# Kernel tuning notes

Measured on AMD Instinct MI355X. Metric: run time of the kernel, lower is better.

Reference implementation:

```python
import jax, jax.numpy as jnp
import numpy as np

B = 65536
NFIELD = 20
NFEAT = 1_000_000
SQL_NEMB = 10
DATA_NEMB = 10
HID = 64
K = 16
C = 2
COL_CARD = NFIELD + NFEAT + 1
GATE_IN = NFIELD * SQL_NEMB
EXP_IN = NFIELD * DATA_NEMB
EPS = 1e-5


def _bn(x, g, b, m, v):
    # eval-mode BatchNorm1d: affine normalize with running stats
    return (x - m) * jax.lax.rsqrt(v + EPS) * g + b


def setup_inputs() -> dict:
    key = jax.random.key(0)
    ks = jax.random.split(key, 12)
    n = lambda k, s, sc=0.05: jax.random.normal(k, s, jnp.float32) * sc
    return {
        "x": jax.random.randint(ks[0], (B, NFIELD), 0, NFEAT, dtype=jnp.int32),
        "sql": jax.random.randint(ks[1], (B, NFIELD), 0, COL_CARD, dtype=jnp.int32),
        "input_table": n(ks[2], (NFEAT, DATA_NEMB)),
        "sql_table": n(ks[3], (COL_CARD, SQL_NEMB)),
        "gate_w1": n(ks[4], (GATE_IN, HID)), "gate_b1": jnp.zeros((HID,), jnp.float32),
        "gate_w2": n(ks[5], (HID, K)), "gate_b2": jnp.zeros((K,), jnp.float32),
        "e_w1": n(ks[6], (K, EXP_IN, HID)), "e_b1": jnp.zeros((K, HID), jnp.float32),
        "e_g1": jnp.ones((K, HID), jnp.float32), "e_beta1": jnp.zeros((K, HID), jnp.float32),
        "e_m1": jnp.zeros((K, HID), jnp.float32), "e_v1": jnp.ones((K, HID), jnp.float32),
        "e_w2": n(ks[7], (K, HID, HID)), "e_b2": jnp.zeros((K, HID), jnp.float32),
        "e_g2": jnp.ones((K, HID), jnp.float32), "e_beta2": jnp.zeros((K, HID), jnp.float32),
        "e_m2": jnp.zeros((K, HID), jnp.float32), "e_v2": jnp.ones((K, HID), jnp.float32),
        "p_w1": n(ks[8], (HID, HID)), "p_b1": jnp.zeros((HID,), jnp.float32),
        "p_g": jnp.ones((HID,), jnp.float32), "p_beta": jnp.zeros((HID,), jnp.float32),
        "p_m": jnp.zeros((HID,), jnp.float32), "p_v": jnp.ones((HID,), jnp.float32),
        "p_w2": n(ks[9], (HID, 1)), "p_b2": jnp.zeros((1,), jnp.float32),
    }


def reference(x, sql, input_table, sql_table, gate_w1, gate_b1, gate_w2, gate_b2,
              e_w1, e_b1, e_g1, e_beta1, e_m1, e_v1,
              e_w2, e_b2, e_g2, e_beta2, e_m2, e_v2,
              p_w1, p_b1, p_g, p_beta, p_m, p_v, p_w2, p_b2):
    Bn = x.shape[0]
    # embedding lookups -> flatten fields
    x_emb = input_table[x].reshape(Bn, -1)      # [B, nfield*data_nemb]
    sql_emb = sql_table[sql].reshape(Bn, -1)    # [B, nfield*sql_nemb]
    # gate network (MLP + softmax) over K experts
    gh = jax.nn.relu(sql_emb @ gate_w1 + gate_b1)
    scores = jax.nn.softmax(gh @ gate_w2 + gate_b2, axis=-1)  # [B, K]
    # sparse top-C selection, scatter back to dense gates, renormalize
    topv, topi = jax.lax.top_k(scores, C)
    gates = jnp.zeros_like(scores).at[jnp.arange(Bn)[:, None], topi].set(topv)
    gates = gates / (gates.sum(-1, keepdims=True) + 1e-9)     # [B, K]
    # expert compute (dense-equivalent; zero gates kill unselected experts)
    h1 = jax.nn.relu(_bn(jnp.einsum('bi,kih->kbh', x_emb, e_w1) + e_b1[:, None, :],
                         e_g1[:, None, :], e_beta1[:, None, :], e_m1[:, None, :], e_v1[:, None, :]))
    h2 = jax.nn.relu(_bn(jnp.einsum('kbh,khg->kbg', h1, e_w2) + e_b2[:, None, :],
                         e_g2[:, None, :], e_beta2[:, None, :], e_m2[:, None, :], e_v2[:, None, :]))
    y = jnp.einsum('bk,kbh->bh', gates, h2)                   # combine [B, HID]
    # load-balance loss: cv^2 of expert importance
    importance = gates.sum(0)
    loss = importance.var() / (importance.mean() ** 2 + 1e-10)
    # predict head
    ph = jax.nn.relu(_bn(y @ p_w1 + p_b1, p_g, p_beta, p_m, p_v))
    out = (ph @ p_w2 + p_b2).squeeze(-1)                      # [B]
    return out, loss
```

## Files before the change

kernel.cpp:

```cpp
#include <hip/hip_runtime.h>
#include <hip/hip_bf16.h>

#define BB 65536
#define NFIELD 20
#define HID 64
#define KEXP 16
#define EPS 1e-5f
#define KPAD 224
#define NKS 7
#define NBLK_GATE 256
#define NBX_EXP 40
#define EMB_BPB 16

typedef __attribute__((ext_vector_type(8))) short v8s;
typedef __attribute__((ext_vector_type(4))) float v4f;

#define OFF_GCNT 0
#define OFF_SC1 64
#define OFF_SH1 1088
#define OFF_SC2 2112
#define OFF_SH2 3136
#define OFF_SCP 4160
#define OFF_SHP 4224
#define OFF_IMP 4288
#define OFF_LIDX 8448
#define OFF_LW  1057024
#define OFF_W1T 2105600
#define OFF_GW1T 2220288
#define OFF_W2T 2227456
#define OFF_PW1T 2260224
#define OFF_XEMB 2262272
#define OFF_SQEMB 9602416
#define OFF_HS 16942448

__device__ __forceinline__ unsigned short f2bf(float f) {
    unsigned int u = __float_as_uint(f);
    unsigned int r = (u + 0x7FFFu + ((u >> 16) & 1u)) >> 16;
    return (unsigned short)r;
}
__device__ __forceinline__ float bf2f(unsigned short u) {
    unsigned int t = ((unsigned int)u) << 16;
    return __uint_as_float(t);
}

__global__ __launch_bounds__(256) void k_prep(
    const float* __restrict__ ew1, const float* __restrict__ ew2,
    const float* __restrict__ gw1, const float* __restrict__ pw1,
    const float* __restrict__ eb1, const float* __restrict__ eg1,
    const float* __restrict__ ebe1, const float* __restrict__ em1,
    const float* __restrict__ ev1,
    const float* __restrict__ eb2, const float* __restrict__ eg2,
    const float* __restrict__ ebe2, const float* __restrict__ em2,
    const float* __restrict__ ev2,
    const float* __restrict__ pb1, const float* __restrict__ pg,
    const float* __restrict__ pbe, const float* __restrict__ pm,
    const float* __restrict__ pv,
    float* __restrict__ wsf, int* __restrict__ gcnt,
    unsigned short* __restrict__ w1t, unsigned short* __restrict__ gw1t,
    unsigned short* __restrict__ w2t, unsigned short* __restrict__ pw1t)
{
    int gid = blockIdx.x * 256 + threadIdx.x;
    if (gid < 229376) {
        int k = gid / 14336, r = gid % 14336, c = r / KPAD, t = r % KPAD;
        w1t[gid] = (t < 200) ? f2bf(ew1[((size_t)k * 200 + t) * HID + c]) : 0;
    } else if (gid < 229376 + 14336) {
        int g2 = gid - 229376; int c = g2 / KPAD, t = g2 % KPAD;
        gw1t[g2] = (t < 200) ? f2bf(gw1[t * HID + c]) : 0;
    } else if (gid < 243712 + 65536) {
        int g2 = gid - 243712; int k = g2 / 4096, r = g2 % 4096, g = r / 64, i = r % 64;
        w2t[g2] = f2bf(ew2[((size_t)k * 64 + i) * 64 + g]);
    } else if (gid < 309248 + 4096) {
        int g2 = gid - 309248; int g = g2 / 64, i = g2 % 64;
        pw1t[g2] = f2bf(pw1[i * 64 + g]);
    } else if (gid < 313344 + 1024) {
        int t = gid - 313344;
        float rs1 = rsqrtf(ev1[t] + EPS) * eg1[t];
        wsf[OFF_SC1 + t] = rs1;
        wsf[OFF_SH1 + t] = fmaf(eb1[t] - em1[t], rs1, ebe1[t]);
        float rs2 = rsqrtf(ev2[t] + EPS) * eg2[t];
        wsf[OFF_SC2 + t] = rs2;
        wsf[OFF_SH2 + t] = fmaf(eb2[t] - em2[t], rs2, ebe2[t]);
    } else if (gid < 314368 + 64) {
        int t = gid - 314368;
        float rs = rsqrtf(pv[t] + EPS) * pg[t];
        wsf[OFF_SCP + t] = rs;
        wsf[OFF_SHP + t] = fmaf(pb1[t] - pm[t], rs, pbe[t]);
    } else if (gid < 314432 + 16) {
        gcnt[gid - 314432] = 0;
    }
}

__global__ __launch_bounds__(256) void k_emb(
    const int* __restrict__ x, const int* __restrict__ sql,
    const float* __restrict__ itab, const float* __restrict__ stab,
    unsigned short* __restrict__ xembT, unsigned short* __restrict__ sqembT)
{
    __shared__ unsigned int lbuf[EMB_BPB * 112];
    int blk = blockIdx.x;
    int sel = blk >= (BB / EMB_BPB);
    int b0 = (sel ? blk - (BB / EMB_BPB) : blk) * EMB_BPB;
    const int* idxp = sel ? sql : x;
    const float* tab = sel ? stab : itab;
    unsigned short* dst = sel ? sqembT : xembT;
    int tid = threadIdx.x;

    if (tid < EMB_BPB * 12)
        lbuf[(tid / 12) * 112 + 100 + (tid % 12)] = 0;

    for (int r = tid; r < EMB_BPB * NFIELD; r += 256) {
        int lb = r / NFIELD, f = r % NFIELD;
        int idx = idxp[b0 * NFIELD + r];
        const float* row = tab + (size_t)idx * 10;
        unsigned int* lrow = &lbuf[lb * 112 + f * 5];
        float2 t0 = *(const float2*)(row + 0);
        float2 t1 = *(const float2*)(row + 2);
        float2 t2 = *(const float2*)(row + 4);
        float2 t3 = *(const float2*)(row + 6);
        float2 t4 = *(const float2*)(row + 8);
        lrow[0] = (unsigned int)f2bf(t0.x) | ((unsigned int)f2bf(t0.y) << 16);
        lrow[1] = (unsigned int)f2bf(t1.x) | ((unsigned int)f2bf(t1.y) << 16);
        lrow[2] = (unsigned int)f2bf(t2.x) | ((unsigned int)f2bf(t2.y) << 16);
        lrow[3] = (unsigned int)f2bf(t3.x) | ((unsigned int)f2bf(t3.y) << 16);
        lrow[4] = (unsigned int)f2bf(t4.x) | ((unsigned int)f2bf(t4.y) << 16);
    }
    __syncthreads();
    uint4* g4 = (uint4*)(dst + (size_t)b0 * KPAD);
    const uint4* l4 = (const uint4*)lbuf;
    g4[tid] = l4[tid];
    if (tid < EMB_BPB * 112 / 4 - 256) g4[256 + tid] = l4[256 + tid];
}

__global__ __launch_bounds__(256, 2) void k_gate(
    const unsigned short* __restrict__ sqembT, const unsigned short* __restrict__ gw1t,
    const float* __restrict__ gb1, const float* __restrict__ gw2,
    const float* __restrict__ gb2,
    int* __restrict__ lidx, float* __restrict__ lw,
    int* __restrict__ gcnt, float* __restrict__ imp_part)
{
    __shared__ unsigned short Hg[4][64][80];
    __shared__ float s_imp[KEXP];
    __shared__ int s_cnt[KEXP];
    __shared__ int s_base[KEXP];
    int tid = threadIdx.x;
    int wid = tid >> 6, l = tid & 63;
    int m = l & 15, q = l >> 4;
    if (tid < KEXP) { s_imp[tid] = 0.f; s_cnt[tid] = 0; }
    __syncthreads();

    int it0 = blockIdx.x * 256 + wid * 64;
    v4f zero4 = {0.f, 0.f, 0.f, 0.f};
    v4f acc[4][4];
#pragma unroll
    for (int a = 0; a < 4; ++a)
#pragma unroll
        for (int c = 0; c < 4; ++c) acc[a][c] = zero4;

    const unsigned short* Ab = sqembT + (size_t)it0 * KPAD + q * 8;
    const unsigned short* Bb = gw1t + m * KPAD + q * 8;
#pragma unroll
    for (int Ks = 0; Ks < NKS; ++Ks) {
        v8s a[4], b[4];
#pragma unroll
        for (int Mt = 0; Mt < 4; ++Mt)
            a[Mt] = *(const v8s*)(Ab + (Mt * 16 + m) * KPAD + Ks * 32);
#pragma unroll
        for (int Nt = 0; Nt < 4; ++Nt)
            b[Nt] = *(const v8s*)(Bb + Nt * 16 * KPAD + Ks * 32);
#pragma unroll
        for (int Mt = 0; Mt < 4; ++Mt)
#pragma unroll
            for (int Nt = 0; Nt < 4; ++Nt)
                acc[Mt][Nt] = __builtin_amdgcn_mfma_f32_16x16x32_bf16(a[Mt], b[Nt], acc[Mt][Nt], 0, 0, 0);
    }
#pragma unroll
    for (int Nt = 0; Nt < 4; ++Nt) {
        int c = Nt * 16 + m;
        float bias = gb1[c];
#pragma unroll
        for (int Mt = 0; Mt < 4; ++Mt)
#pragma unroll
            for (int j = 0; j < 4; ++j) {
                int item = Mt * 16 + q * 4 + j;
                float v = fmaxf(acc[Mt][Nt][j] + bias, 0.f);
                Hg[wid][item][c ^ ((item & 7) << 3)] = f2bf(v);
            }
    }
    float z[KEXP];
#pragma unroll
    for (int j = 0; j < KEXP; ++j) z[j] = gb2[j];
#pragma unroll
    for (int u = 0; u < 8; ++u) {
        v8s hv = *(const v8s*)&Hg[wid][l][(u * 8) ^ ((l & 7) << 3)];
#pragma unroll
        for (int e = 0; e < 8; ++e) {
            int h = u * 8 + e;
            float g = bf2f((unsigned short)hv[e]);
#pragma unroll
            for (int j = 0; j < KEXP; ++j) z[j] = fmaf(g, gw2[h * KEXP + j], z[j]);
        }
    }
    float mm = z[0];
#pragma unroll
    for (int j = 1; j < KEXP; ++j) mm = fmaxf(mm, z[j]);
    float s = 0.f;
#pragma unroll
    for (int j = 0; j < KEXP; ++j) s += expf(z[j] - mm);
    int i0 = 0; float m0 = z[0];
#pragma unroll
    for (int j = 1; j < KEXP; ++j) if (z[j] > m0) { m0 = z[j]; i0 = j; }
    int i1 = (i0 == 0) ? 1 : 0; float m1 = -3.4e38f;
#pragma unroll
    for (int j = 0; j < KEXP; ++j) if (j != i0 && z[j] > m1) { m1 = z[j]; i1 = j; }
    float v0 = expf(m0 - mm) / s, v1 = expf(m1 - mm) / s;
    float inv = 1.f / (v0 + v1 + 1e-9f);
    float w0 = v0 * inv, w1 = v1 * inv;

    int b = blockIdx.x * 256 + tid;
    atomicAdd(&s_imp[i0], w0);
    atomicAdd(&s_imp[i1], w1);
    int o0 = atomicAdd(&s_cnt[i0], 1);
    int o1 = atomicAdd(&s_cnt[i1], 1);
    __syncthreads();
    if (tid < KEXP) {
        imp_part[blockIdx.x * KEXP + tid] = s_imp[tid];
        s_base[tid] = atomicAdd(&gcnt[tid], s_cnt[tid]);
    }
    __syncthreads();
    int p0 = i0 * BB + s_base[i0] + o0;
    lidx[p0] = (b << 1);     lw[p0] = w0;
    int p1 = i1 * BB + s_base[i1] + o1;
    lidx[p1] = (b << 1) | 1; lw[p1] = w1;
}

__global__ void k_pad(const int* __restrict__ gcnt, int* __restrict__ lidx,
                      float* __restrict__ lw)
{
    int k = blockIdx.x;
    int n = gcnt[k];
    int ne = (n + 63) & ~63;
    for (int i = n + threadIdx.x; i < ne; i += 64) {
        lidx[k * BB + i] = 2 * BB;
        lw[k * BB + i] = 0.f;
    }
}

__global__ __launch_bounds__(256) void k_loss(const float* __restrict__ imp_part,
                                              float* __restrict__ out)
{
    __shared__ double sred[16][17];
    __shared__ double simp[KEXP];
    int tid = threadIdx.x;
    int j = tid & 15, g = tid >> 4;
    double s = 0.0;
    for (int blk = g; blk < NBLK_GATE; blk += 16) s += (double)imp_part[blk * KEXP + j];
    sred[g][j] = s;
    __syncthreads();
    if (tid < KEXP) {
        double t = 0.0;
#pragma unroll
        for (int gg = 0; gg < 16; ++gg) t += sred[gg][tid];
        simp[tid] = t;
    }
    __syncthreads();
    if (tid == 0) {
        double mean = 0.0;
        for (int jj = 0; jj < KEXP; ++jj) mean += simp[jj];
        mean /= KEXP;
        double var = 0.0;
        for (int jj = 0; jj < KEXP; ++jj) { double d = simp[jj] - mean; var += d * d; }
        var /= KEXP;
        out[BB] = (float)(var / (mean * mean + 1e-10));
    }
}

__global__ __launch_bounds__(256, 2) void k_exp(
    const unsigned short* __restrict__ xembT,
    const unsigned short* __restrict__ w1t, const unsigned short* __restrict__ w2t,
    const float* __restrict__ sc1, const float* __restrict__ sh1,
    const float* __restrict__ sc2, const float* __restrict__ sh2,
    const int* __restrict__ lidx, const float* __restrict__ lw,
    const int* __restrict__ gcnt, unsigned short* __restrict__ hs)
{
    __shared__ unsigned short Hl[4][64][80];
    int k = blockIdx.y;
    int tid = threadIdx.x;
    int wid = tid >> 6, l = tid & 63;
    int m = l & 15, q = l >> 4;
    int n = gcnt[k];
    int ne = (n + 63) & ~63;
    const unsigned short* W1 = w1t + (size_t)k * 64 * KPAD + m * KPAD + q * 8;
    const unsigned short* W2 = w2t + (size_t)k * 64 * 64 + m * 64 + q * 8;
    float sc1v[4], sh1v[4], sc2v[4], sh2v[4];
#pragma unroll
    for (int Nt = 0; Nt < 4; ++Nt) {
        int c = Nt * 16 + m;
        sc1v[Nt] = sc1[k * HID + c]; sh1v[Nt] = sh1[k * HID + c];
        sc2v[Nt] = sc2[k * HID + c]; sh2v[Nt] = sh2[k * HID + c];
    }
    v4f zero4 = {0.f, 0.f, 0.f, 0.f};

    for (int it0 = (blockIdx.x * 4 + wid) * 64; it0 < ne; it0 += NBX_EXP * 256) {
        int eA[4];
#pragma unroll
        for (int Mt = 0; Mt < 4; ++Mt) eA[Mt] = lidx[k * BB + it0 + Mt * 16 + m];
        v4f acc1[4][4];
#pragma unroll
        for (int a = 0; a < 4; ++a)
#pragma unroll
            for (int c = 0; c < 4; ++c) acc1[a][c] = zero4;
#pragma unroll
        for (int Ks = 0; Ks < NKS; ++Ks) {
            v8s a[4], b[4];
#pragma unroll
            for (int Mt = 0; Mt < 4; ++Mt)
                a[Mt] = *(const v8s*)(xembT + (size_t)(eA[Mt] >> 1) * KPAD + Ks * 32 + q * 8);
#pragma unroll
            for (int Nt = 0; Nt < 4; ++Nt)
                b[Nt] = *(const v8s*)(W1 + Nt * 16 * KPAD + Ks * 32);
#pragma unroll
            for (int Mt = 0; Mt < 4; ++Mt)
#pragma unroll
                for (int Nt = 0; Nt < 4; ++Nt)
                    acc1[Mt][Nt] = __builtin_amdgcn_mfma_f32_16x16x32_bf16(a[Mt], b[Nt], acc1[Mt][Nt], 0, 0, 0);
        }
#pragma unroll
        for (int Nt = 0; Nt < 4; ++Nt) {
            int c = Nt * 16 + m;
#pragma unroll
            for (int Mt = 0; Mt < 4; ++Mt)
#pragma unroll
                for (int j = 0; j < 4; ++j) {
                    int item = Mt * 16 + q * 4 + j;
                    float v = fmaxf(fmaf(acc1[Mt][Nt][j], sc1v[Nt], sh1v[Nt]), 0.f);
                    Hl[wid][item][c ^ ((item & 7) << 3)] = f2bf(v);
                }
        }
        v4f acc2[4][4];
#pragma unroll
        for (int a = 0; a < 4; ++a)
#pragma unroll
            for (int c = 0; c < 4; ++c) acc2[a][c] = zero4;
#pragma unroll
        for (int Ks = 0; Ks < 2; ++Ks) {
            v8s a[4], b[4];
#pragma unroll
            for (int Mt = 0; Mt < 4; ++Mt)
                a[Mt] = *(const v8s*)&Hl[wid][Mt * 16 + m][(Ks * 32 + q * 8) ^ ((m & 7) << 3)];
#pragma unroll
            for (int Nt = 0; Nt < 4; ++Nt)
                b[Nt] = *(const v8s*)(W2 + Nt * 16 * 64 + Ks * 32);
#pragma unroll
            for (int Mt = 0; Mt < 4; ++Mt)
#pragma unroll
                for (int Nt = 0; Nt < 4; ++Nt)
                    acc2[Mt][Nt] = __builtin_amdgcn_mfma_f32_16x16x32_bf16(a[Mt], b[Nt], acc2[Mt][Nt], 0, 0, 0);
        }
#pragma unroll
        for (int Mt = 0; Mt < 4; ++Mt) {
            float4 wC = *(const float4*)&lw[k * BB + it0 + Mt * 16 + q * 4];
            float wj[4] = {wC.x, wC.y, wC.z, wC.w};
#pragma unroll
            for (int Nt = 0; Nt < 4; ++Nt) {
                int c = Nt * 16 + m;
#pragma unroll
                for (int j = 0; j < 4; ++j) {
                    int item = Mt * 16 + q * 4 + j;
                    float v = wj[j] * fmaxf(fmaf(acc2[Mt][Nt][j], sc2v[Nt], sh2v[Nt]), 0.f);
                    Hl[wid][item][c ^ ((item & 7) << 3)] = f2bf(v);
                }
            }
        }
        int eo = lidx[k * BB + it0 + l];
        unsigned short* hrow = hs + (size_t)eo * HID;
#pragma unroll
        for (int u = 0; u < 8; ++u)
            *(v8s*)(hrow + u * 8) = *(const v8s*)&Hl[wid][l][(u * 8) ^ ((l & 7) << 3)];
    }
}

__global__ __launch_bounds__(256, 2) void k_head(
    const unsigned short* __restrict__ hs, const unsigned short* __restrict__ pw1t,
    const float* __restrict__ scp, const float* __restrict__ shp,
    const float* __restrict__ pw2, const float* __restrict__ pb2,
    float* __restrict__ out)
{
    int tid = threadIdx.x;
    int wid = tid >> 6, l = tid & 63;
    int m = l & 15, q = l >> 4;
    int it0 = blockIdx.x * 256 + wid * 64;
    float scv[4], shv[4], w2v[4];
#pragma unroll
    for (int Nt = 0; Nt < 4; ++Nt) {
        int c = Nt * 16 + m;
        scv[Nt] = scp[c]; shv[Nt] = shp[c]; w2v[Nt] = pw2[c];
    }
    v4f zero4 = {0.f, 0.f, 0.f, 0.f};
    v4f acc[4][4];
#pragma unroll
    for (int a = 0; a < 4; ++a)
#pragma unroll
        for (int c = 0; c < 4; ++c) acc[a][c] = zero4;

#pragma unroll
    for (int Ks = 0; Ks < 2; ++Ks) {
        v8s a[4], b[4];
#pragma unroll
        for (int Mt = 0; Mt < 4; ++Mt) {
            int bi = it0 + Mt * 16 + m;
            const unsigned short* r0 = hs + (size_t)(2 * bi) * HID + Ks * 32 + q * 8;
            v8s u0 = *(const v8s*)r0;
            v8s u1 = *(const v8s*)(r0 + HID);
            v8s av;
#pragma unroll
            for (int e = 0; e < 8; ++e) {
                float f = bf2f((unsigned short)u0[e]) + bf2f((unsigned short)u1[e]);
                av[e] = (short)f2bf(f);
            }
            a[Mt] = av;
        }
#pragma unroll
        for (int Nt = 0; Nt < 4; ++Nt)
            b[Nt] = *(const v8s*)(pw1t + (Nt * 16 + m) * HID + Ks * 32 + q * 8);
#pragma unroll
        for (int Mt = 0; Mt < 4; ++Mt)
#pragma unroll
            for (int Nt = 0; Nt < 4; ++Nt)
                acc[Mt][Nt] = __builtin_amdgcn_mfma_f32_16x16x32_bf16(a[Mt], b[Nt], acc[Mt][Nt], 0, 0, 0);
    }
    float pb2v = pb2[0];
#pragma unroll
    for (int Mt = 0; Mt < 4; ++Mt) {
#pragma unroll
        for (int j = 0; j < 4; ++j) {
            float po = 0.f;
#pragma unroll
            for (int Nt = 0; Nt < 4; ++Nt) {
                float ph = fmaxf(fmaf(acc[Mt][Nt][j], scv[Nt], shv[Nt]), 0.f);
                po = fmaf(ph, w2v[Nt], po);
            }
            po += __shfl_xor(po, 1);
            po += __shfl_xor(po, 2);
            po += __shfl_xor(po, 4);
            po += __shfl_xor(po, 8);
            if (m == 0) out[it0 + Mt * 16 + q * 4 + j] = po + pb2v;
        }
    }
}

extern "C" void kernel_launch(void* const* d_in, const int* in_sizes, int n_in,
                              void* d_out, int out_size, void* d_ws, size_t ws_size,
                              hipStream_t stream) {
    const int*   x     = (const int*)d_in[0];
    const int*   sql   = (const int*)d_in[1];
    const float* itab  = (const float*)d_in[2];
    const float* stab  = (const float*)d_in[3];
    const float* gw1   = (const float*)d_in[4];
    const float* gb1   = (const float*)d_in[5];
    const float* gw2   = (const float*)d_in[6];
    const float* gb2   = (const float*)d_in[7];
    const float* ew1   = (const float*)d_in[8];
    const float* eb1   = (const float*)d_in[9];
    const float* eg1   = (const float*)d_in[10];
    const float* ebe1  = (const float*)d_in[11];
    const float* em1   = (const float*)d_in[12];
    const float* ev1   = (const float*)d_in[13];
    const float* ew2   = (const float*)d_in[14];
    const float* eb2   = (const float*)d_in[15];
    const float* eg2   = (const float*)d_in[16];
    const float* ebe2  = (const float*)d_in[17];
    const float* em2   = (const float*)d_in[18];
    const float* ev2   = (const float*)d_in[19];
    const float* pw1   = (const float*)d_in[20];
    const float* pb1   = (const float*)d_in[21];
    const float* pg    = (const float*)d_in[22];
    const float* pbe   = (const float*)d_in[23];
    const float* pm    = (const float*)d_in[24];
    const float* pv    = (const float*)d_in[25];
    const float* pw2   = (const float*)d_in[26];
    const float* pb2   = (const float*)d_in[27];

    float* wsf = (float*)d_ws;
    int*   wsi = (int*)d_ws;
    int*   gcnt = wsi + OFF_GCNT;
    float* sc1 = wsf + OFF_SC1;
    float* sh1 = wsf + OFF_SH1;
    float* sc2 = wsf + OFF_SC2;
    float* sh2 = wsf + OFF_SH2;
    float* scp = wsf + OFF_SCP;
    float* shp = wsf + OFF_SHP;
    float* imp = wsf + OFF_IMP;
    int*   lidx = wsi + OFF_LIDX;
    float* lw  = wsf + OFF_LW;
    unsigned short* w1t   = (unsigned short*)(wsf + OFF_W1T);
    unsigned short* gw1t  = (unsigned short*)(wsf + OFF_GW1T);
    unsigned short* w2t   = (unsigned short*)(wsf + OFF_W2T);
    unsigned short* pw1t  = (unsigned short*)(wsf + OFF_PW1T);
    unsigned short* xembT = (unsigned short*)(wsf + OFF_XEMB);
    unsigned short* sqembT= (unsigned short*)(wsf + OFF_SQEMB);
    unsigned short* hs    = (unsigned short*)(wsf + OFF_HS);
    float* out = (float*)d_out;

    k_prep<<<1229, 256, 0, stream>>>(ew1, ew2, gw1, pw1,
                                     eb1, eg1, ebe1, em1, ev1,
                                     eb2, eg2, ebe2, em2, ev2,
                                     pb1, pg, pbe, pm, pv,
                                     wsf, gcnt, w1t, gw1t, w2t, pw1t);
    k_emb<<<2 * (BB / EMB_BPB), 256, 0, stream>>>(x, sql, itab, stab, xembT, sqembT);
    k_gate<<<NBLK_GATE, 256, 0, stream>>>(sqembT, gw1t, gb1, gw2, gb2,
                                          lidx, lw, gcnt, imp);
    k_loss<<<1, 256, 0, stream>>>(imp, out);
    k_pad<<<16, 64, 0, stream>>>(gcnt, lidx, lw);
    dim3 ge(NBX_EXP, KEXP);
    k_exp<<<ge, 256, 0, stream>>>(xembT, w1t, w2t, sc1, sh1, sc2, sh2,
                                  lidx, lw, gcnt, hs);
    k_head<<<256, 256, 0, stream>>>(hs, pw1t, scp, shp, pw2, pb2, out);
}
```

Measured before the change: 153.2 us.

## Fuse SQL embedding gather into gate kernel and drop sqembT buffer

The SQL-table embedding gather moves out of k_emb and into k_gate. Each gate block now gathers its own 64 rows into a shared-memory tile and runs the MFMA GEMM from LDS. Each wave computes 16 hidden columns instead of 64 items, and the grid grows to 1024 blocks. This removes the global write and read-back of the bf16 sqembT intermediate, at the cost of a gather-bound prologue in the gate kernel, a single wave doing softmax/top-k per block, and barriers placed inside divergent branches.

```diff
diff --git a/kernel.cpp b/kernel.cpp
--- a/kernel.cpp
+++ b/kernel.cpp
@@ -8,9 +8,10 @@
 #define EPS 1e-5f
 #define KPAD 224
 #define NKS 7
-#define NBLK_GATE 256
+#define NBLK_GATE 1024
 #define NBX_EXP 40
 #define EMB_BPB 16
+#define TSTR 228
 
 typedef __attribute__((ext_vector_type(8))) short v8s;
 typedef __attribute__((ext_vector_type(4))) float v4f;
@@ -23,15 +24,14 @@
 #define OFF_SCP 4160
 #define OFF_SHP 4224
 #define OFF_IMP 4288
-#define OFF_LIDX 8448
-#define OFF_LW  1057024
-#define OFF_W1T 2105600
-#define OFF_GW1T 2220288
-#define OFF_W2T 2227456
-#define OFF_PW1T 2260224
-#define OFF_XEMB 2262272
-#define OFF_SQEMB 9602416
-#define OFF_HS 16942448
+#define OFF_LIDX 20672
+#define OFF_LW  1069248
+#define OFF_W1T 2117824
+#define OFF_GW1T 2232512
+#define OFF_W2T 2239680
+#define OFF_PW1T 2272448
+#define OFF_XEMB 2274496
+#define OFF_HS 9614640
 
 __device__ __forceinline__ unsigned short f2bf(float f) {
     unsigned int u = __float_as_uint(f);
@@ -91,17 +91,11 @@
 }
 
 __global__ __launch_bounds__(256) void k_emb(
-    const int* __restrict__ x, const int* __restrict__ sql,
-    const float* __restrict__ itab, const float* __restrict__ stab,
-    unsigned short* __restrict__ xembT, unsigned short* __restrict__ sqembT)
+    const int* __restrict__ x, const float* __restrict__ itab,
+    unsigned short* __restrict__ xembT)
 {
     __shared__ unsigned int lbuf[EMB_BPB * 112];
-    int blk = blockIdx.x;
-    int sel = blk >= (BB / EMB_BPB);
-    int b0 = (sel ? blk - (BB / EMB_BPB) : blk) * EMB_BPB;
-    const int* idxp = sel ? sql : x;
-    const float* tab = sel ? stab : itab;
-    unsigned short* dst = sel ? sqembT : xembT;
+    int b0 = blockIdx.x * EMB_BPB;
     int tid = threadIdx.x;
 
     if (tid < EMB_BPB * 12)
@@ -109,8 +103,8 @@
 
     for (int r = tid; r < EMB_BPB * NFIELD; r += 256) {
         int lb = r / NFIELD, f = r % NFIELD;
-        int idx = idxp[b0 * NFIELD + r];
-        const float* row = tab + (size_t)idx * 10;
+        int idx = x[b0 * NFIELD + r];
+        const float* row = itab + (size_t)idx * 10;
         unsigned int* lrow = &lbuf[lb * 112 + f * 5];
         float2 t0 = *(const float2*)(row + 0);
         float2 t1 = *(const float2*)(row + 2);
@@ -124,112 +118,134 @@
         lrow[4] = (unsigned int)f2bf(t4.x) | ((unsigned int)f2bf(t4.y) << 16);
     }
     __syncthreads();
-    uint4* g4 = (uint4*)(dst + (size_t)b0 * KPAD);
+    uint4* g4 = (uint4*)(xembT + (size_t)b0 * KPAD);
     const uint4* l4 = (const uint4*)lbuf;
     g4[tid] = l4[tid];
     if (tid < EMB_BPB * 112 / 4 - 256) g4[256 + tid] = l4[256 + tid];
 }
 
-__global__ __launch_bounds__(256, 2) void k_gate(
-    const unsigned short* __restrict__ sqembT, const unsigned short* __restrict__ gw1t,
+__global__ __launch_bounds__(256) void k_gate(
+    const int* __restrict__ sql, const float* __restrict__ stab,
+    const unsigned short* __restrict__ gw1t,
     const float* __restrict__ gb1, const float* __restrict__ gw2,
     const float* __restrict__ gb2,
     int* __restrict__ lidx, float* __restrict__ lw,
     int* __restrict__ gcnt, float* __restrict__ imp_part)
 {
-    __shared__ unsigned short Hg[4][64][80];
+    __shared__ unsigned short tile[64][TSTR];
     __shared__ float s_imp[KEXP];
     __shared__ int s_cnt[KEXP];
     __shared__ int s_base[KEXP];
+    unsigned short (*Hg)[80] = (unsigned short (*)[80])&tile[0][0];
     int tid = threadIdx.x;
     int wid = tid >> 6, l = tid & 63;
     int m = l & 15, q = l >> 4;
+    int b0 = blockIdx.x * 64;
+
     if (tid < KEXP) { s_imp[tid] = 0.f; s_cnt[tid] = 0; }
-    __syncthreads();
-
-    int it0 = blockIdx.x * 256 + wid * 64;
+    for (int t = tid; t < 64 * 12; t += 256) {
+        int r = t / 12, c2 = t % 12;
+        *(unsigned int*)&tile[r][200 + 2 * c2] = 0;
+    }
+#pragma unroll
+    for (int rr = 0; rr < 5; ++rr) {
+        int r = tid + rr * 256;
+        int lb = r / NFIELD, f = r % NFIELD;
+        int idx = sql[(size_t)(b0 + lb) * NFIELD + f];
+        const float* row = stab + (size_t)idx * 10;
+        float2 t0 = *(const float2*)(row + 0);
+        float2 t1 = *(const float2*)(row + 2);
+        float2 t2 = *(const float2*)(row + 4);
+        float2 t3 = *(const float2*)(row + 6);
+        float2 t4 = *(const float2*)(row + 8);
+        unsigned int* lrow = (unsigned int*)&tile[lb][f * 10];
+        lrow[0] = (unsigned int)f2bf(t0.x) | ((unsigned int)f2bf(t0.y) << 16);
+        lrow[1] = (unsigned int)f2bf(t1.x) | ((unsigned int)f2bf(t1.y) << 16);
+        lrow[2] = (unsigned int)f2bf(t2.x) | ((unsigned int)f2bf(t2.y) << 16);
+        lrow[3] = (unsigned int)f2bf(t3.x) | ((unsigned int)f2bf(t3.y) << 16);
+        lrow[4] = (unsigned int)f2bf(t4.x) | ((unsigned int)f2bf(t4.y) << 16);
+    }
+    __syncthreads();
+
     v4f zero4 = {0.f, 0.f, 0.f, 0.f};
-    v4f acc[4][4];
-#pragma unroll
-    for (int a = 0; a < 4; ++a)
-#pragma unroll
-        for (int c = 0; c < 4; ++c) acc[a][c] = zero4;
-
-    const unsigned short* Ab = sqembT + (size_t)it0 * KPAD + q * 8;
-    const unsigned short* Bb = gw1t + m * KPAD + q * 8;
+    v4f acc[4];
+#pragma unroll
+    for (int a = 0; a < 4; ++a) acc[a] = zero4;
+    const unsigned short* Bb = gw1t + (wid * 16 + m) * KPAD + q * 8;
 #pragma unroll
     for (int Ks = 0; Ks < NKS; ++Ks) {
-        v8s a[4], b[4];
+        v8s bv = *(const v8s*)(Bb + Ks * 32);
+        v8s a[4];
 #pragma unroll
         for (int Mt = 0; Mt < 4; ++Mt)
-            a[Mt] = *(const v8s*)(Ab + (Mt * 16 + m) * KPAD + Ks * 32);
-#pragma unroll
-        for (int Nt = 0; Nt < 4; ++Nt)
-            b[Nt] = *(const v8s*)(Bb + Nt * 16 * KPAD + Ks * 32);
+            a[Mt] = *(const v8s*)&tile[Mt * 16 + m][Ks * 32 + q * 8];
 #pragma unroll
         for (int Mt = 0; Mt < 4; ++Mt)
-#pragma unroll
-            for (int Nt = 0; Nt < 4; ++Nt)
-                acc[Mt][Nt] = __builtin_amdgcn_mfma_f32_16x16x32_bf16(a[Mt], b[Nt], acc[Mt][Nt], 0, 0, 0);
-    }
-#pragma unroll
-    for (int Nt = 0; Nt < 4; ++Nt) {
-        int c = Nt * 16 + m;
-        float bias = gb1[c];
-#pragma unroll
-        for (int Mt = 0; Mt < 4; ++Mt)
-#pragma unroll
-            for (int j = 0; j < 4; ++j) {
-                int item = Mt * 16 + q * 4 + j;
-                float v = fmaxf(acc[Mt][Nt][j] + bias, 0.f);
-                Hg[wid][item][c ^ ((item & 7) << 3)] = f2bf(v);
+            acc[Mt] = __builtin_amdgcn_mfma_f32_16x16x32_bf16(a[Mt], bv, acc[Mt], 0, 0, 0);
+    }
+    __syncthreads();
+
+    int c = wid * 16 + m;
+    float bias = gb1[c];
+#pragma unroll
+    for (int Mt = 0; Mt < 4; ++Mt)
+#pragma unroll
+        for (int j = 0; j < 4; ++j) {
+            int item = Mt * 16 + q * 4 + j;
+            float v = fmaxf(acc[Mt][j] + bias, 0.f);
+            Hg[item][c ^ ((item & 7) << 3)] = f2bf(v);
+        }
+    __syncthreads();
+
+    if (wid == 0) {
+        float z[KEXP];
+#pragma unroll
+        for (int j = 0; j < KEXP; ++j) z[j] = gb2[j];
+#pragma unroll
+        for (int u = 0; u < 8; ++u) {
+            v8s hv = *(const v8s*)&Hg[l][(u * 8) ^ ((l & 7) << 3)];
+#pragma unroll
+            for (int e = 0; e < 8; ++e) {
+                int h = u * 8 + e;
+                float g = bf2f((unsigned short)hv[e]);
+#pragma unroll
+                for (int j = 0; j < KEXP; ++j) z[j] = fmaf(g, gw2[h * KEXP + j], z[j]);
             }
-    }
-    float z[KEXP];
-#pragma unroll
-    for (int j = 0; j < KEXP; ++j) z[j] = gb2[j];
-#pragma unroll
-    for (int u = 0; u < 8; ++u) {
-        v8s hv = *(const v8s*)&Hg[wid][l][(u * 8) ^ ((l & 7) << 3)];
-#pragma unroll
-        for (int e = 0; e < 8; ++e) {
-            int h = u * 8 + e;
-            float g = bf2f((unsigned short)hv[e]);
-#pragma unroll
-            for (int j = 0; j < KEXP; ++j) z[j] = fmaf(g, gw2[h * KEXP + j], z[j]);
-        }
-    }
-    float mm = z[0];
-#pragma unroll
-    for (int j = 1; j < KEXP; ++j) mm = fmaxf(mm, z[j]);
-    float s = 0.f;
-#pragma unroll
-    for (int j = 0; j < KEXP; ++j) s += expf(z[j] - mm);
-    int i0 = 0; float m0 = z[0];
-#pragma unroll
-    for (int j = 1; j < KEXP; ++j) if (z[j] > m0) { m0 = z[j]; i0 = j; }
-    int i1 = (i0 == 0) ? 1 : 0; float m1 = -3.4e38f;
-#pragma unroll
-    for (int j = 0; j < KEXP; ++j) if (j != i0 && z[j] > m1) { m1 = z[j]; i1 = j; }
-    float v0 = expf(m0 - mm) / s, v1 = expf(m1 - mm) / s;
-    float inv = 1.f / (v0 + v1 + 1e-9f);
-    float w0 = v0 * inv, w1 = v1 * inv;
-
-    int b = blockIdx.x * 256 + tid;
-    atomicAdd(&s_imp[i0], w0);
-    atomicAdd(&s_imp[i1], w1);
-    int o0 = atomicAdd(&s_cnt[i0], 1);
-    int o1 = atomicAdd(&s_cnt[i1], 1);
-    __syncthreads();
-    if (tid < KEXP) {
-        imp_part[blockIdx.x * KEXP + tid] = s_imp[tid];
-        s_base[tid] = atomicAdd(&gcnt[tid], s_cnt[tid]);
-    }
-    __syncthreads();
-    int p0 = i0 * BB + s_base[i0] + o0;
-    lidx[p0] = (b << 1);     lw[p0] = w0;
-    int p1 = i1 * BB + s_base[i1] + o1;
-    lidx[p1] = (b << 1) | 1; lw[p1] = w1;
+        }
+        float mm = z[0];
+#pragma unroll
+        for (int j = 1; j < KEXP; ++j) mm = fmaxf(mm, z[j]);
+        float s = 0.f;
+#pragma unroll
+        for (int j = 0; j < KEXP; ++j) s += expf(z[j] - mm);
+        int i0 = 0; float m0 = z[0];
+#pragma unroll
+        for (int j = 1; j < KEXP; ++j) if (z[j] > m0) { m0 = z[j]; i0 = j; }
+        int i1 = (i0 == 0) ? 1 : 0; float m1 = -3.4e38f;
+#pragma unroll
+        for (int j = 0; j < KEXP; ++j) if (j != i0 && z[j] > m1) { m1 = z[j]; i1 = j; }
+        float v0 = expf(m0 - mm) / s, v1 = expf(m1 - mm) / s;
+        float inv = 1.f / (v0 + v1 + 1e-9f);
+        float w0 = v0 * inv, w1 = v1 * inv;
+
+        atomicAdd(&s_imp[i0], w0);
+        atomicAdd(&s_imp[i1], w1);
+        int o0 = atomicAdd(&s_cnt[i0], 1);
+        int o1 = atomicAdd(&s_cnt[i1], 1);
+        __syncthreads();
+        if (l < KEXP) s_base[l] = atomicAdd(&gcnt[l], s_cnt[l]);
+        __syncthreads();
+        int b = b0 + l;
+        int p0 = i0 * BB + s_base[i0] + o0;
+        lidx[p0] = (b << 1);     lw[p0] = w0;
+        int p1 = i1 * BB + s_base[i1] + o1;
+        lidx[p1] = (b << 1) | 1; lw[p1] = w1;
+    } else {
+        __syncthreads();
+        __syncthreads();
+    }
+    __syncthreads();
+    if (tid < KEXP) imp_part[blockIdx.x * KEXP + tid] = s_imp[tid];
 }
 
 __global__ void k_pad(const int* __restrict__ gcnt, int* __restrict__ lidx,
@@ -496,7 +512,6 @@
     unsigned short* w2t   = (unsigned short*)(wsf + OFF_W2T);
     unsigned short* pw1t  = (unsigned short*)(wsf + OFF_PW1T);
     unsigned short* xembT = (unsigned short*)(wsf + OFF_XEMB);
-    unsigned short* sqembT= (unsigned short*)(wsf + OFF_SQEMB);
     unsigned short* hs    = (unsigned short*)(wsf + OFF_HS);
     float* out = (float*)d_out;
 
@@ -505,8 +520,8 @@
                                      eb2, eg2, ebe2, em2, ev2,
                                      pb1, pg, pbe, pm, pv,
                                      wsf, gcnt, w1t, gw1t, w2t, pw1t);
-    k_emb<<<2 * (BB / EMB_BPB), 256, 0, stream>>>(x, sql, itab, stab, xembT, sqembT);
-    k_gate<<<NBLK_GATE, 256, 0, stream>>>(sqembT, gw1t, gb1, gw2, gb2,
+    k_emb<<<BB / EMB_BPB, 256, 0, stream>>>(x, itab, xembT);
+    k_gate<<<NBLK_GATE, 256, 0, stream>>>(sql, stab, gw1t, gb1, gw2, gb2,
                                           lidx, lw, gcnt, imp);
     k_loss<<<1, 256, 0, stream>>>(imp, out);
     k_pad<<<16, 64, 0, stream>>>(gcnt, lidx, lw);
```

After: 150.9 us. No clear change (-1.5%).
